# Optimization experiments

Measured on AMD Instinct MI355X. Metric: run time of the kernel, lower is better.

The kernel has to match this reference:

```python
import jax, jax.numpy as jnp
import numpy as np

N_STATE = 16
PNAMES = ['in_w', 'conv_w', 'conv_b', 'xproj_w', 'dt_w', 'dt_b', 'A_log', 'D', 'ln_g', 'ln_b', 'out_w']


def _ss2d_params(key, dm, K):
    di = 2 * dm                       # expand = 2
    dr = (dm + 15) // 16              # dt_rank = ceil(d_model/16)
    ks = jax.random.split(key, 6)
    s = lambda k, shape, sc: jax.random.normal(k, shape, jnp.float32) * sc
    cshape = (di, 1, 3, 3) if K == 4 else (di, 1, 3)   # depthwise conv kernel
    return {
        'in_w': s(ks[0], (2 * di, dm), dm ** -0.5),
        'conv_w': s(ks[1], cshape, 0.3),
        'conv_b': jnp.zeros((di,), jnp.float32),
        'xproj_w': s(ks[2], (K, dr + 2 * N_STATE, di), di ** -0.5),
        'dt_w': s(ks[3], (K, di, dr), dr ** -0.5),
        'dt_b': s(ks[4], (K, di), 0.1),
        'A_log': jnp.log(jnp.arange(1, N_STATE + 1, dtype=jnp.float32)) * jnp.ones((K, di, N_STATE), jnp.float32),
        'D': jnp.ones((K, di), jnp.float32),
        'ln_g': jnp.ones((di,), jnp.float32),
        'ln_b': jnp.zeros((di,), jnp.float32),
        'out_w': s(ks[5], (dm, di), di ** -0.5),
    }


def _ln(x, g, b, eps=1e-5):
    m = jnp.mean(x, -1, keepdims=True)
    v = jnp.mean((x - m) ** 2, -1, keepdims=True)
    return (x - m) * jax.lax.rsqrt(v + eps) * g + b


def _scan_branches(xs, p):
    # xs: (B, K, di, L) -- selective scan along L for each direction k
    dr = p['dt_w'].shape[-1]
    x_dbl = jnp.einsum('bkdl,kcd->bkcl', xs, p['xproj_w'])
    dts, Bs, Cs = jnp.split(x_dbl, [dr, dr + N_STATE], axis=2)
    delta = jax.nn.softplus(jnp.einsum('bkrl,kdr->bkdl', dts, p['dt_w']) + p['dt_b'][None, :, :, None])
    A = -jnp.exp(p['A_log'])                               # (K, di, N)
    dA = jnp.exp(jnp.einsum('bkdl,kdn->lbkdn', delta, A))  # time-major for scan
    dBu = jnp.einsum('bkdl,bknl,bkdl->lbkdn', delta, Bs, xs)

    def step(h, io):
        a, bu = io
        h = a * h + bu
        return h, h

    h0 = jnp.zeros(dA.shape[1:], xs.dtype)
    _, hs = jax.lax.scan(step, h0, (dA, dBu))              # (L, B, K, di, N)
    y = jnp.einsum('lbkdn,bknl->bkdl', hs, Cs)
    return y + xs * p['D'][None, :, :, None]


def _ss2d_2d(x, p):
    # VMamba SS2D: x (B, H, W, dm) -> (B, H, W, dm), 4 scan directions
    xz = jnp.einsum('bhwc,ec->bhwe', x, p['in_w'])
    xin, z = jnp.split(xz, 2, -1)
    u = xin.transpose(0, 3, 1, 2)
    u = jax.lax.conv_general_dilated(u, p['conv_w'], (1, 1), 'SAME',
        dimension_numbers=('NCHW', 'OIHW', 'NCHW'), feature_group_count=u.shape[1])
    u = jax.nn.silu(u + p['conv_b'][None, :, None, None])
    Bb, di, H, W = u.shape
    L = H * W
    xf = u.reshape(Bb, di, L)                              # row-major
    xt = u.transpose(0, 1, 3, 2).reshape(Bb, di, L)        # col-major
    xs = jnp.stack([xf, xt, xf[..., ::-1], xt[..., ::-1]], 1)
    ys = _scan_branches(xs, p)                             # (B, 4, di, L)
    y0 = ys[:, 0]
    y2 = ys[:, 2][..., ::-1]
    y1 = ys[:, 1].reshape(Bb, di, W, H).transpose(0, 1, 3, 2).reshape(Bb, di, L)
    y3 = ys[:, 3][..., ::-1].reshape(Bb, di, W, H).transpose(0, 1, 3, 2).reshape(Bb, di, L)
    y = (y0 + y1 + y2 + y3).transpose(0, 2, 1).reshape(Bb, H, W, di)
    y = _ln(y, p['ln_g'], p['ln_b']) * jax.nn.silu(z)
    return jnp.einsum('bhwe,ce->bhwc', y, p['out_w'])


def _ss2d_1d(x, p):
    # SS2D_xb fuse block: x (B, L, dm) -> (B, L, dm), bidirectional 1D scan
    xz = jnp.einsum('blc,ec->ble', x, p['in_w'])
    xin, z = jnp.split(xz, 2, -1)
    u = xin.transpose(0, 2, 1)
    u = jax.lax.conv_general_dilated(u, p['conv_w'], (1,), 'SAME',
        dimension_numbers=('NCH', 'OIH', 'NCH'), feature_group_count=u.shape[1])
    u = jax.nn.silu(u + p['conv_b'][None, :, None])
    xs = jnp.stack([u, u[..., ::-1]], 1)                   # K = 2
    ys = _scan_branches(xs, p)
    y = (ys[:, 0] + ys[:, 1][..., ::-1]).transpose(0, 2, 1)
    y = _ln(y, p['ln_g'], p['ln_b']) * jax.nn.silu(z)
    return jnp.einsum('ble,ce->blc', y, p['out_w'])


def _bridge(C1, C2, C3, p1, p2, p3, pf, n1_g, n1_b):
    y1 = _ss2d_2d(C1.transpose(0, 2, 3, 1), p1).transpose(0, 3, 1, 2)
    y2 = _ss2d_2d(C2.transpose(0, 2, 3, 1), p2).transpose(0, 3, 1, 2)
    y3 = _ss2d_2d(C3.transpose(0, 2, 3, 1), p3).transpose(0, 3, 1, 2)
    B_, C, H, W = y1.shape                                 # C=24, H=W=112
    # faithful RAW reshapes (no permute), exactly as the torch source does
    F1 = y1.reshape(B_, H * W, C)
    F2 = y2.reshape(B_, H * W // 2, C)
    F3 = y3.reshape(B_, H * W // 4, C)
    F = jnp.concatenate([F1, F2, F3], axis=1)              # (B, 21952, 24)
    F = F + _ss2d_1d(_ln(F, n1_g, n1_b), pf)               # dropout = identity (eval)
    o1 = F[:, :12544, :].reshape(B_, C, H, W)
    o2 = F[:, 12544:18816, :].reshape(B_, C * 2, H // 2, W // 2)
    o3 = F[:, 18816:, :].reshape(B_, C * 4, H // 4, W // 4)
    return (o1, o2, o3)


def setup_inputs() -> dict:
    key = jax.random.key(0)
    ks = jax.random.split(key, 7)
    inp = {
        'C1': jax.random.normal(ks[0], (1, 24, 112, 112), jnp.float32),
        'C2': jax.random.normal(ks[1], (1, 48, 56, 56), jnp.float32),
        'C3': jax.random.normal(ks[2], (1, 96, 28, 28), jnp.float32),
    }
    for pfx, dm, K, kk in [('m1', 24, 4, ks[3]), ('m2', 48, 4, ks[4]), ('m3', 96, 4, ks[5]), ('fz', 24, 2, ks[6])]:
        p = _ss2d_params(kk, dm, K)
        for n in PNAMES:
            inp[pfx + '_' + n] = p[n]
    inp['n1_g'] = jnp.ones((24,), jnp.float32)
    inp['n1_b'] = jnp.zeros((24,), jnp.float32)
    return inp


def reference(C1, C2, C3, m1_in_w, m1_conv_w, m1_conv_b, m1_xproj_w, m1_dt_w, m1_dt_b, m1_A_log, m1_D, m1_ln_g, m1_ln_b, m1_out_w, m2_in_w, m2_conv_w, m2_conv_b, m2_xproj_w, m2_dt_w, m2_dt_b, m2_A_log, m2_D, m2_ln_g, m2_ln_b, m2_out_w, m3_in_w, m3_conv_w, m3_conv_b, m3_xproj_w, m3_dt_w, m3_dt_b, m3_A_log, m3_D, m3_ln_g, m3_ln_b, m3_out_w, fz_in_w, fz_conv_w, fz_conv_b, fz_xproj_w, fz_dt_w, fz_dt_b, fz_A_log, fz_D, fz_ln_g, fz_ln_b, fz_out_w, n1_g, n1_b):
    p1 = dict(zip(PNAMES, (m1_in_w, m1_conv_w, m1_conv_b, m1_xproj_w, m1_dt_w, m1_dt_b, m1_A_log, m1_D, m1_ln_g, m1_ln_b, m1_out_w)))
    p2 = dict(zip(PNAMES, (m2_in_w, m2_conv_w, m2_conv_b, m2_xproj_w, m2_dt_w, m2_dt_b, m2_A_log, m2_D, m2_ln_g, m2_ln_b, m2_out_w)))
    p3 = dict(zip(PNAMES, (m3_in_w, m3_conv_w, m3_conv_b, m3_xproj_w, m3_dt_w, m3_dt_b, m3_A_log, m3_D, m3_ln_g, m3_ln_b, m3_out_w)))
    pf = dict(zip(PNAMES, (fz_in_w, fz_conv_w, fz_conv_b, fz_xproj_w, fz_dt_w, fz_dt_b, fz_A_log, fz_D, fz_ln_g, fz_ln_b, fz_out_w)))
    return _bridge(C1, C2, C3, p1, p2, p3, pf, n1_g, n1_b)
```

## Files before the change

kernel.cpp:

```cpp
#include <hip/hip_runtime.h>
#include <hip/hip_bf16.h>
#include <hip/hip_fp16.h>

#define NST 16
#define L2E 1.4426950408889634f

typedef const void* inp;
typedef __half h16;

struct Job {
  inp Cin;
  inp in_w, conv_w, conv_b, xproj_w, dt_w, dt_b, A_log, D, ln_g, ln_b, out_w;
  h16 *u_pre, *z, *u, *delta, *Bs, *Cs, *yg;
  h16 *Hc;
  float *yacc, *Wc, *bc, *Ssum, *A2t, *F0out;
  float *outF; const float* resid;
  const int* aflg;
  int dm, di, dr, K, H, W, L, NCH, CLEN, is2d, TL, CG, PT, cinf;
};
struct Jobs { Job j[4]; int n; const int* dtf; };

__device__ __forceinline__ float ldw(inp p, size_t i, int f32){
  return f32 ? ((const float*)p)[i]
             : __bfloat162float(((const __hip_bfloat16*)p)[i]);
}
__device__ __forceinline__ float hf(const h16* p, size_t i){ return __half2float(p[i]); }
__device__ __forceinline__ float sigm(float x){ return 1.0f/(1.0f + __expf(-x)); }
__device__ __forceinline__ float silu_(float x){ return x * sigm(x); }
__device__ __forceinline__ float softp(float x){ return (x > 20.0f) ? x : __logf(1.0f + __expf(x)); }

__device__ __forceinline__ int map_pos(const Job& J, int k, int l){
  int rev   = J.is2d ? (k >= 2) : (k == 1);
  int trans = J.is2d ? (k & 1) : 0;
  int sl = rev ? (J.L - 1 - l) : l;
  return trans ? ((sl % J.H)*J.W + sl / J.H) : sl;
}

union F4H { float4 f; __half2 h[4]; };

__device__ __forceinline__ void ld16v(const h16* p, float* o){
  const float4* q = (const float4*)p;
  F4H a, b; a.f = q[0]; b.f = q[1];
  #pragma unroll
  for (int i = 0; i < 4; i++){ float2 x = __half22float2(a.h[i]); o[2*i] = x.x; o[2*i+1] = x.y; }
  #pragma unroll
  for (int i = 0; i < 4; i++){ float2 x = __half22float2(b.h[i]); o[8+2*i] = x.x; o[8+2*i+1] = x.y; }
}

__device__ __forceinline__ void ld8v(const h16* p, float* o){
  F4H a; a.f = *(const float4*)p;
  #pragma unroll
  for (int i = 0; i < 4; i++){ float2 x = __half22float2(a.h[i]); o[2*i] = x.x; o[2*i+1] = x.y; }
}

__device__ __forceinline__ void cvt16(float4 a4, float4 b4, float* o){
  F4H a, b; a.f = a4; b.f = b4;
  #pragma unroll
  for (int i = 0; i < 4; i++){ float2 x = __half22float2(a.h[i]); o[2*i] = x.x; o[2*i+1] = x.y; }
  #pragma unroll
  for (int i = 0; i < 4; i++){ float2 x = __half22float2(b.h[i]); o[8+2*i] = x.x; o[8+2*i+1] = x.y; }
}


__global__ void k_detect(const unsigned* D1, int* flag, int* afl){
  if (blockIdx.x == 0){
    if (threadIdx.x == 0) flag[0] = (D1[0] == 0x3F800000u) ? 1 : 0;
    if (threadIdx.x < 4) afl[threadIdx.x] = 1;
  }
}

__global__ void k_wcomb(Jobs js){
  int f32 = *js.dtf;
  int b = blockIdx.x;
  for (int m = 0; m < js.n; m++){
    const Job& J = js.j[m];
    int CC = J.di + 2*NST;
    int CC2 = CC + NST;
    int tot = J.K * CC2 * J.di;
    int nb = (tot + 255) >> 8;
    if (b < nb){
      int t = (b << 8) + (int)threadIdx.x;
      if (t < tot){
        int d = t % J.di; int r = t / J.di; int cout = r % CC2; int k = r / CC2;
        if (cout < J.di){
          float v = 0.0f;
          for (int rr = 0; rr < J.dr; rr++)
            v += ldw(J.dt_w, (size_t)(k*J.di + cout)*J.dr + rr, f32) *
                 ldw(J.xproj_w, (size_t)(k*(J.dr + 2*NST) + rr)*J.di + d, f32);
          J.Wc[(size_t)(k*CC + cout)*J.di + d] = v;
          if (d == 0) J.bc[k*CC + cout] = ldw(J.dt_b, k*J.di + cout, f32);
        } else if (cout < CC){
          int nn = cout - J.di;
          J.Wc[(size_t)(k*CC + cout)*J.di + d] =
            ldw(J.xproj_w, (size_t)(k*(J.dr + 2*NST) + J.dr + nn)*J.di + d, f32);
          if (d == 0) J.bc[k*CC + cout] = 0.0f;
        } else {
          int nn = cout - CC;
          float v = -L2E*__expf(ldw(J.A_log, ((size_t)(k*J.di + d) << 4) + nn, f32));
          J.A2t[(size_t)(k*NST + nn)*J.di + d] = v;
          float base = -L2E*__expf(ldw(J.A_log, ((size_t)(k*J.di + d) << 4), f32));
          float expect = (float)(nn+1)*base;
          if (fabsf(v - expect) > 1e-4f*fabsf(expect) + 1e-6f)
            atomicAnd((int*)J.aflg, 0);
        }
      }
      return;
    }
    b -= nb;
  }
}

__global__ void k_inproj(Jobs js){
  int f32 = *js.dtf;
  int b = blockIdx.x;
  for (int m = 0; m < js.n; m++){
    const Job& J = js.j[m];
    int tot = 2*J.di*J.L;
    int nb = (tot + 255) >> 8;
    if (b < nb){
      int cf = J.cinf ? 1 : f32;
      int t = (b << 8) + (int)threadIdx.x;
      if (t < tot){
        int p = t % J.L; int e = t / J.L;
        float acc;
        if (cf && f32){
          const float* Ci = (const float*)J.Cin;
          const float4* w4 = (const float4*)((const float*)J.in_w + (size_t)e*J.dm);
          float a0 = 0.f, a1 = 0.f, a2 = 0.f, a3 = 0.f;
          int n4 = J.dm >> 2;
          for (int c4 = 0; c4 < n4; c4++){
            float4 w = w4[c4];
            int c = c4 << 2;
            a0 = fmaf(Ci[(size_t)(c+0)*J.L + p], w.x, a0);
            a1 = fmaf(Ci[(size_t)(c+1)*J.L + p], w.y, a1);
            a2 = fmaf(Ci[(size_t)(c+2)*J.L + p], w.z, a2);
            a3 = fmaf(Ci[(size_t)(c+3)*J.L + p], w.w, a3);
          }
          acc = (a0+a1)+(a2+a3);
        } else {
          float a0 = 0.f, a1 = 0.f, a2 = 0.f, a3 = 0.f;
          for (int c = 0; c < J.dm; c += 4){
            a0 = fmaf(ldw(J.Cin, (size_t)(c+0)*J.L + p, cf), ldw(J.in_w, (size_t)e*J.dm + c+0, f32), a0);
            a1 = fmaf(ldw(J.Cin, (size_t)(c+1)*J.L + p, cf), ldw(J.in_w, (size_t)e*J.dm + c+1, f32), a1);
            a2 = fmaf(ldw(J.Cin, (size_t)(c+2)*J.L + p, cf), ldw(J.in_w, (size_t)e*J.dm + c+2, f32), a2);
            a3 = fmaf(ldw(J.Cin, (size_t)(c+3)*J.L + p, cf), ldw(J.in_w, (size_t)e*J.dm + c+3, f32), a3);
          }
          acc = (a0+a1)+(a2+a3);
        }
        if (e < J.di) J.u_pre[(size_t)p*J.di + e] = __float2half(acc);
        else          J.z[(size_t)p*J.di + (e - J.di)] = __float2half(acc);
      }
      return;
    }
    b -= nb;
  }
}

__global__ __launch_bounds__(256) void k_lnproj(const float* F0, inp g, inp bb, inp in_w,
                                                h16* u_pre, h16* z, int L, const int* dtf){
  __shared__ float xr[64][25];
  __shared__ float wsmT[24*96];
  int f32 = *dtf;
  int p0 = blockIdx.x << 6;
  int rows = L - p0; if (rows > 64) rows = 64;
  for (int i = threadIdx.x; i < 24*96; i += 256){
    int c = i / 96, e = i % 96;
    wsmT[i] = ldw(in_w, (size_t)e*24 + c, f32);
  }
  for (int idx = threadIdx.x; idx < rows*24; idx += 256){
    int r = idx / 24, c = idx % 24;
    xr[r][c] = F0[(size_t)(p0 + r)*24 + c];
  }
  __syncthreads();
  if ((int)threadIdx.x < rows){
    float* row = xr[threadIdx.x];
    float s = 0.f;
    #pragma unroll
    for (int c = 0; c < 24; c++) s += row[c];
    float mean = s * (1.0f/24.0f);
    float s2 = 0.f;
    #pragma unroll
    for (int c = 0; c < 24; c++){ float t = row[c]-mean; s2 = fmaf(t,t,s2); }
    float rs = rsqrtf(s2*(1.0f/24.0f) + 1e-5f);
    #pragma unroll
    for (int c = 0; c < 24; c++)
      row[c] = (row[c]-mean)*rs*ldw(g,c,f32) + ldw(bb,c,f32);
  }
  __syncthreads();
  for (int idx = threadIdx.x; idx < rows*96; idx += 256){
    int r = idx / 96, e = idx % 96;
    const float* row = xr[r];
    float acc = 0.f;
    #pragma unroll
    for (int c = 0; c < 24; c++) acc = fmaf(row[c], wsmT[c*96 + e], acc);
    if (e < 48) u_pre[(size_t)(p0+r)*48 + e] = __float2half(acc);
    else        z[(size_t)(p0+r)*48 + (e-48)] = __float2half(acc);
  }
}

__global__ void k_conv(Jobs js){
  int f32 = *js.dtf;
  int b = blockIdx.x;
  for (int m = 0; m < js.n; m++){
    const Job& J = js.j[m];
    int tot = J.L * J.di;
    int nb = (tot + 255) >> 8;
    if (b < nb){
      int t = (b << 8) + (int)threadIdx.x;
      if (t < tot){
        int d = t % J.di; int p = t / J.di;
        float acc = ldw(J.conv_b, d, f32);
        if (J.is2d){
          int h = p / J.W, w = p % J.W;
          for (int kh = 0; kh < 3; kh++){
            int hh = h + kh - 1;
            if ((unsigned)hh < (unsigned)J.H){
              for (int kw = 0; kw < 3; kw++){
                int ww = w + kw - 1;
                if ((unsigned)ww < (unsigned)J.W)
                  acc += ldw(J.conv_w, d*9 + kh*3 + kw, f32) * hf(J.u_pre, (size_t)(hh*J.W + ww)*J.di + d);
              }
            }
          }
        } else {
          for (int kk = 0; kk < 3; kk++){
            int pp = p + kk - 1;
            if ((unsigned)pp < (unsigned)J.L)
              acc += ldw(J.conv_w, d*3 + kk, f32) * hf(J.u_pre, (size_t)pp*J.di + d);
          }
        }
        J.u[(size_t)p*J.di + d] = __float2half(silu_(acc));
      }
      return;
    }
    b -= nb;
  }
}

__global__ void k_deltaBC(Jobs js){
  extern __shared__ float xt[];
  int b = blockIdx.x;
  for (int m = 0; m < js.n; m++){
    const Job& J = js.j[m];
    int TL = J.TL;
    int ntile = (J.L + TL - 1)/TL;
    int nb = J.K * ntile;
    if (b < nb){
      int k = b / ntile, tile = b % ntile;
      int l0 = tile * TL;
      int stride = J.di + 4;
      int d8n = J.di >> 3;
      int VE = TL * d8n;
      for (int idx = threadIdx.x; idx < VE; idx += 256){
        int ll = idx / d8n, d8 = idx % d8n;
        int l = l0 + ll;
        float o[8];
        if (l < J.L){
          ld8v(J.u + (size_t)map_pos(J, k, l)*J.di + (d8 << 3), o);
        } else {
          for (int i = 0; i < 8; i++) o[i] = 0.0f;
        }
        float4* dst = (float4*)(xt + ll*stride + (d8 << 3));
        dst[0] = make_float4(o[0],o[1],o[2],o[3]);
        dst[1] = make_float4(o[4],o[5],o[6],o[7]);
      }
      __syncthreads();
      int CC = J.di + 2*NST;
      int c4n = CC >> 2;
      int NL4 = TL >> 2;
      int items = NL4 * c4n;
      int n4 = J.di >> 2;
      for (int item = threadIdx.x; item < items; item += 256){
        int l4 = item % NL4;
        int cbase = (item / NL4) << 2;
        const float4* w0 = (const float4*)(J.Wc + (size_t)(k*CC + cbase+0)*J.di);
        const float4* w1 = (const float4*)(J.Wc + (size_t)(k*CC + cbase+1)*J.di);
        const float4* w2 = (const float4*)(J.Wc + (size_t)(k*CC + cbase+2)*J.di);
        const float4* w3 = (const float4*)(J.Wc + (size_t)(k*CC + cbase+3)*J.di);
        const float4* x0 = (const float4*)(xt + (l4 + 0*NL4)*stride);
        const float4* x1 = (const float4*)(xt + (l4 + 1*NL4)*stride);
        const float4* x2 = (const float4*)(xt + (l4 + 2*NL4)*stride);
        const float4* x3 = (const float4*)(xt + (l4 + 3*NL4)*stride);
        float acc[4][4];
        #pragma unroll
        for (int j = 0; j < 4; j++){
          acc[j][0]=0.f; acc[j][1]=0.f; acc[j][2]=0.f; acc[j][3]=0.f;
        }
        #pragma unroll 4
        for (int d4 = 0; d4 < n4; d4++){
          float4 W0 = w0[d4], W1 = w1[d4], W2 = w2[d4], W3 = w3[d4];
          float4 X0 = x0[d4], X1 = x1[d4], X2 = x2[d4], X3 = x3[d4];
          #define DOT4(a,X,W) { a = fmaf(X.x,W.x,a); a = fmaf(X.y,W.y,a); a = fmaf(X.z,W.z,a); a = fmaf(X.w,W.w,a); }
          DOT4(acc[0][0],X0,W0) DOT4(acc[0][1],X0,W1) DOT4(acc[0][2],X0,W2) DOT4(acc[0][3],X0,W3)
          DOT4(acc[1][0],X1,W0) DOT4(acc[1][1],X1,W1) DOT4(acc[1][2],X1,W2) DOT4(acc[1][3],X1,W3)
          DOT4(acc[2][0],X2,W0) DOT4(acc[2][1],X2,W1) DOT4(acc[2][2],X2,W2) DOT4(acc[2][3],X2,W3)
          DOT4(acc[3][0],X3,W0) DOT4(acc[3][1],X3,W1) DOT4(acc[3][2],X3,W2) DOT4(acc[3][3],X3,W3)
          #undef DOT4
        }
        float b0 = J.bc[k*CC + cbase+0], b1 = J.bc[k*CC + cbase+1];
        float b2 = J.bc[k*CC + cbase+2], b3 = J.bc[k*CC + cbase+3];
        #pragma unroll
        for (int j = 0; j < 4; j++){
          int l = l0 + l4 + NL4*j;
          if (l >= J.L) continue;
          float av[4] = {acc[j][0]+b0, acc[j][1]+b1, acc[j][2]+b2, acc[j][3]+b3};
          #pragma unroll
          for (int i = 0; i < 4; i++){
            int cout = cbase + i; float v = av[i];
            if (cout < J.di)            J.delta[((size_t)k*J.L + l)*J.di + cout] = __float2half(softp(v));
            else if (cout < J.di + NST) J.Bs[((size_t)k*J.L + l)*NST + (cout - J.di)] = __float2half(v);
            else                        J.Cs[((size_t)k*J.L + l)*NST + (cout - J.di - NST)] = __float2half(v);
          }
        }
      }
      return;
    }
    b -= nb;
  }
}

#define STEPRQ { if (rev){ if(--rm < 0){ rm = J.H - 1; qd--; } } else { if(++rm == J.H){ rm = 0; qd++; } } }

#define HUPD_GEN(S, DX, B) { \
  _Pragma("unroll") \
  for (int n = 0; n < NST; n++) h[n] = fmaf(exp2f((S) * A2[n]), h[n], (DX) * (B)[n]); }
#define HUPDY_GEN(S, DX, B, C, Y) { \
  _Pragma("unroll") \
  for (int n = 0; n < NST; n++){ h[n] = fmaf(exp2f((S) * A2[n]), h[n], (DX) * (B)[n]); (Y) = fmaf(h[n], (C)[n], (Y)); } }

#define POWTREE(Q, P) \
  float P[NST]; \
  P[0]=(Q); P[1]=P[0]*P[0]; P[2]=P[1]*P[0]; P[3]=P[1]*P[1]; \
  P[4]=P[3]*P[0]; P[5]=P[3]*P[1]; P[6]=P[3]*P[2]; P[7]=P[3]*P[3]; \
  P[8]=P[7]*P[0]; P[9]=P[7]*P[1]; P[10]=P[7]*P[2]; P[11]=P[7]*P[3]; \
  P[12]=P[7]*P[4]; P[13]=P[7]*P[5]; P[14]=P[7]*P[6]; P[15]=P[7]*P[7];

#define HUPD_POW(S, DX, B) { \
  float q_ = exp2f((S) * A0); \
  POWTREE(q_, Pw) \
  _Pragma("unroll") \
  for (int n = 0; n < NST; n++) h[n] = fmaf(Pw[n], h[n], (DX) * (B)[n]); }
#define HUPDY_POW(S, DX, B, C, Y) { \
  float q_ = exp2f((S) * A0); \
  POWTREE(q_, Pw) \
  _Pragma("unroll") \
  for (int n = 0; n < NST; n++){ h[n] = fmaf(Pw[n], h[n], (DX) * (B)[n]); (Y) = fmaf(h[n], (C)[n], (Y)); } }

__global__ __launch_bounds__(256) void k_passA(Jobs js){
  int b = blockIdx.x;
  int wid = (int)threadIdx.x >> 6;
  int lane = (int)threadIdx.x & 63;
  for (int m = 0; m < js.n; m++){
    const Job& J = js.j[m];
    int DG = (J.di + 63) >> 6;
    int units = J.K * J.NCH * DG;
    int nb = (units + 3) >> 2;
    if (b < nb){
      int uu = (b << 2) + wid;
      if (uu >= units) return;
      int afl = *J.aflg;
      int k = uu / (J.NCH * DG);
      int r = uu % (J.NCH * DG);
      int chunk = r / DG, dg = r % DG;
      int d = (dg << 6) + lane;
      if (d >= J.di) return;
      int c0 = chunk * J.CLEN;
      int c1 = c0 + J.CLEN; if (c1 > J.L) c1 = J.L;
      size_t sb = (size_t)(k*J.NCH + chunk);
      if (c0 >= J.L){
        J.Ssum[sb*J.di + d] = 0.0f;
        #pragma unroll
        for (int n = 0; n < NST; n++) J.Hc[(sb*NST + n)*J.di + d] = __float2half(0.0f);
        return;
      }
      float h[NST];
      #pragma unroll
      for (int n = 0; n < NST; n++) h[n] = 0.0f;
      float ss = 0.0f;
      int rev   = J.is2d ? (k >= 2) : (k == 1);
      int trans = J.is2d ? (k & 1) : 0;
      int rm = 0, qd = 0;
      if (trans){
        int sl0 = rev ? (J.L - 1 - c0) : c0;
        qd = sl0 / J.H; rm = sl0 % J.H;
      }
      const h16* dlt = J.delta + ((size_t)k*J.L)*J.di + d;
      const h16* Bb  = J.Bs + ((size_t)k*J.L)*NST;
      if (afl){
        float A0 = J.A2t[(size_t)(k*NST)*J.di + d];
        int l = c0;
        int pos0;
        h16 s0h, s1h, x0h, x1h;
        float4 B0a, B0b, B1a, B1b;
        if (trans){ pos0 = rm*J.W + qd; STEPRQ; } else pos0 = rev ? (J.L-1-l) : l;
        s0h = dlt[(size_t)l*J.di];
        x0h = J.u[(size_t)pos0*J.di + d];
        { const float4* bp = (const float4*)(Bb + (size_t)l*NST); B0a = bp[0]; B0b = bp[1]; }
        s1h = s0h; x1h = x0h; B1a = B0a; B1b = B0b;
        if (l + 1 < c1){
          int pos1;
          if (trans){ pos1 = rm*J.W + qd; STEPRQ; } else pos1 = rev ? (J.L-2-l) : (l+1);
          s1h = dlt[(size_t)(l+1)*J.di];
          x1h = J.u[(size_t)pos1*J.di + d];
          const float4* bq = (const float4*)(Bb + (size_t)(l+1)*NST); B1a = bq[0]; B1b = bq[1];
        }
        while (l < c1){
          int ln = l + 2;
          h16 ns0 = s0h, ns1 = s1h, nx0 = x0h, nx1 = x1h;
          float4 nB0a = B0a, nB0b = B0b, nB1a = B1a, nB1b = B1b;
          if (ln < c1){
            int np0;
            if (trans){ np0 = rm*J.W + qd; STEPRQ; } else np0 = rev ? (J.L-1-ln) : ln;
            ns0 = dlt[(size_t)ln*J.di];
            nx0 = J.u[(size_t)np0*J.di + d];
            const float4* bp = (const float4*)(Bb + (size_t)ln*NST); nB0a = bp[0]; nB0b = bp[1];
            if (ln + 1 < c1){
              int np1;
              if (trans){ np1 = rm*J.W + qd; STEPRQ; } else np1 = rev ? (J.L-2-ln) : (ln+1);
              ns1 = dlt[(size_t)(ln+1)*J.di];
              nx1 = J.u[(size_t)np1*J.di + d];
              const float4* bq = (const float4*)(Bb + (size_t)(ln+1)*NST); nB1a = bq[0]; nB1b = bq[1];
            }
          }
          {
            float s0 = __half2float(s0h), x0 = __half2float(x0h);
            float B0[NST]; cvt16(B0a, B0b, B0);
            float dx0 = s0 * x0; ss += s0;
            HUPD_POW(s0, dx0, B0)
            if (l + 1 < c1){
              float s1 = __half2float(s1h), x1 = __half2float(x1h);
              float B1[NST]; cvt16(B1a, B1b, B1);
              float dx1 = s1 * x1; ss += s1;
              HUPD_POW(s1, dx1, B1)
            }
          }
          l = ln;
          s0h = ns0; s1h = ns1; x0h = nx0; x1h = nx1;
          B0a = nB0a; B0b = nB0b; B1a = nB1a; B1b = nB1b;
        }
      } else {
        float A2[NST];
        #pragma unroll
        for (int n = 0; n < NST; n++) A2[n] = J.A2t[(size_t)(k*NST + n)*J.di + d];
        for (int l = c0; l < c1; l++){
          int pos;
          if (trans){ pos = rm*J.W + qd; STEPRQ; } else pos = rev ? (J.L-1-l) : l;
          float s0 = hf(dlt, (size_t)l*J.di);
          float x0 = hf(J.u, (size_t)pos*J.di + d);
          float B0[NST]; ld16v(Bb + (size_t)l*NST, B0);
          float dx0 = s0 * x0; ss += s0;
          HUPD_GEN(s0, dx0, B0)
        }
      }
      J.Ssum[sb*J.di + d] = ss;
      #pragma unroll
      for (int n = 0; n < NST; n++)
        J.Hc[(sb*NST + n)*J.di + d] = __float2half(h[n]);
      return;
    }
    b -= nb;
  }
}

__global__ __launch_bounds__(1024) void k_passB(Jobs js){
  __shared__ float sA[64*17], sH[64*17];
  int b = blockIdx.x;
  int sid = (int)threadIdx.x >> 4;
  int dd  = (int)threadIdx.x & 15;
  for (int m = 0; m < js.n; m++){
    const Job& J = js.j[m];
    int DT = J.di >> 4;
    int nb = J.K * NST * DT;
    if (b < nb){
      int k  = b / (NST*DT);
      int r  = b % (NST*DT);
      int n  = r / DT;
      int dt = r % DT;
      int d = dt*16 + dd;
      int SL = J.NCH >> 6;
      int c0 = sid*SL, c1 = c0 + SL;
      float An = J.A2t[(size_t)(k*NST + n)*J.di + d];
      float a = 1.0f, hagg = 0.0f;
      {
        size_t rb = (size_t)(k*J.NCH + c0);
        float ss = J.Ssum[rb*J.di + d];
        h16 hch  = J.Hc[(rb*NST + n)*J.di + d];
        for (int c = c0; c < c1; c++){
          float ssc = ss; h16 hcc = hch;
          if (c + 1 < c1){
            size_t rn = (size_t)(k*J.NCH + c + 1);
            ss  = J.Ssum[rn*J.di + d];
            hch = J.Hc[(rn*NST + n)*J.di + d];
          }
          float P = exp2f(An * ssc);
          hagg = fmaf(P, hagg, __half2float(hcc));
          a *= P;
        }
      }
      sA[sid*17+dd] = a; sH[sid*17+dd] = hagg;
      __syncthreads();
      #pragma unroll
      for (int s = 1; s < 64; s <<= 1){
        float pa = 1.0f, ph = 0.0f;
        if (sid >= s){ pa = sA[(sid-s)*17+dd]; ph = sH[(sid-s)*17+dd]; }
        __syncthreads();
        hagg = fmaf(a, ph, hagg);
        a *= pa;
        sA[sid*17+dd] = a; sH[sid*17+dd] = hagg;
        __syncthreads();
      }
      float Hp = (sid == 0) ? 0.0f : sH[(sid-1)*17+dd];
      {
        size_t rb = (size_t)(k*J.NCH + c0);
        float ss = J.Ssum[rb*J.di + d];
        h16 hch  = J.Hc[(rb*NST + n)*J.di + d];
        for (int c = c0; c < c1; c++){
          float ssc = ss; float hc = __half2float(hch);
          size_t idx = ((size_t)(k*J.NCH + c)*NST + n)*J.di + d;
          if (c + 1 < c1){
            size_t rn = (size_t)(k*J.NCH + c + 1);
            ss  = J.Ssum[rn*J.di + d];
            hch = J.Hc[(rn*NST + n)*J.di + d];
          }
          float P = exp2f(An * ssc);
          J.Hc[idx] = __float2half(Hp);
          Hp = fmaf(P, Hp, hc);
        }
      }
      return;
    }
    b -= nb;
  }
}

__global__ __launch_bounds__(256) void k_passC(Jobs js){
  int f32 = *js.dtf;
  int b = blockIdx.x;
  int wid = (int)threadIdx.x >> 6;
  int lane = (int)threadIdx.x & 63;
  for (int m = 0; m < js.n; m++){
    const Job& J = js.j[m];
    int DG = (J.di + 63) >> 6;
    int units = J.K * J.NCH * DG;
    int nb = (units + 3) >> 2;
    if (b < nb){
      int uu = (b << 2) + wid;
      if (uu >= units) return;
      int afl = *J.aflg;
      int k = uu / (J.NCH * DG);
      int r = uu % (J.NCH * DG);
      int chunk = r / DG, dg = r % DG;
      int d = (dg << 6) + lane;
      if (d >= J.di) return;
      int c0 = chunk * J.CLEN;
      int c1 = c0 + J.CLEN; if (c1 > J.L) c1 = J.L;
      if (c0 >= J.L) return;
      float h[NST];
      size_t sb = (size_t)(k*J.NCH + chunk);
      #pragma unroll
      for (int n = 0; n < NST; n++) h[n] = hf(J.Hc, (sb*NST + n)*J.di + d);
      float Dd = ldw(J.D, k*J.di + d, f32);
      float* yk = J.yacc + (size_t)k*J.L*J.di;
      int rev   = J.is2d ? (k >= 2) : (k == 1);
      int trans = J.is2d ? (k & 1) : 0;
      int rm = 0, qd = 0;
      if (trans){
        int sl0 = rev ? (J.L - 1 - c0) : c0;
        qd = sl0 / J.H; rm = sl0 % J.H;
      }
      const h16* dlt = J.delta + ((size_t)k*J.L)*J.di + d;
      const h16* Bb  = J.Bs + ((size_t)k*J.L)*NST;
      const h16* Cb  = J.Cs + ((size_t)k*J.L)*NST;
      if (afl){
        float A0 = J.A2t[(size_t)(k*NST)*J.di + d];
        int l = c0;
        int pos0, pos1 = 0;
        h16 s0h, s1h, x0h, x1h;
        float4 B0a, B0b, B1a, B1b, C0a, C0b, C1a, C1b;
        if (trans){ pos0 = rm*J.W + qd; STEPRQ; } else pos0 = rev ? (J.L-1-l) : l;
        s0h = dlt[(size_t)l*J.di];
        x0h = J.u[(size_t)pos0*J.di + d];
        { const float4* bp = (const float4*)(Bb + (size_t)l*NST); B0a = bp[0]; B0b = bp[1];
          const float4* cp = (const float4*)(Cb + (size_t)l*NST); C0a = cp[0]; C0b = cp[1]; }
        s1h = s0h; x1h = x0h; B1a = B0a; B1b = B0b; C1a = C0a; C1b = C0b;
        if (l + 1 < c1){
          if (trans){ pos1 = rm*J.W + qd; STEPRQ; } else pos1 = rev ? (J.L-2-l) : (l+1);
          s1h = dlt[(size_t)(l+1)*J.di];
          x1h = J.u[(size_t)pos1*J.di + d];
          const float4* bq = (const float4*)(Bb + (size_t)(l+1)*NST); B1a = bq[0]; B1b = bq[1];
          const float4* cq = (const float4*)(Cb + (size_t)(l+1)*NST); C1a = cq[0]; C1b = cq[1];
        }
        while (l < c1){
          int ln = l + 2;
          int np0 = pos0, np1 = pos1;
          h16 ns0 = s0h, ns1 = s1h, nx0 = x0h, nx1 = x1h;
          float4 nB0a = B0a, nB0b = B0b, nB1a = B1a, nB1b = B1b;
          float4 nC0a = C0a, nC0b = C0b, nC1a = C1a, nC1b = C1b;
          if (ln < c1){
            if (trans){ np0 = rm*J.W + qd; STEPRQ; } else np0 = rev ? (J.L-1-ln) : ln;
            ns0 = dlt[(size_t)ln*J.di];
            nx0 = J.u[(size_t)np0*J.di + d];
            { const float4* bp = (const float4*)(Bb + (size_t)ln*NST); nB0a = bp[0]; nB0b = bp[1];
              const float4* cp = (const float4*)(Cb + (size_t)ln*NST); nC0a = cp[0]; nC0b = cp[1]; }
            if (ln + 1 < c1){
              if (trans){ np1 = rm*J.W + qd; STEPRQ; } else np1 = rev ? (J.L-2-ln) : (ln+1);
              ns1 = dlt[(size_t)(ln+1)*J.di];
              nx1 = J.u[(size_t)np1*J.di + d];
              const float4* bq = (const float4*)(Bb + (size_t)(ln+1)*NST); nB1a = bq[0]; nB1b = bq[1];
              const float4* cq = (const float4*)(Cb + (size_t)(ln+1)*NST); nC1a = cq[0]; nC1b = cq[1];
            }
          }
          {
            float s0 = __half2float(s0h), x0 = __half2float(x0h);
            float B0[NST], C0[NST]; cvt16(B0a, B0b, B0); cvt16(C0a, C0b, C0);
            float dx0 = s0 * x0;
            float y0 = 0.0f;
            HUPDY_POW(s0, dx0, B0, C0, y0)
            y0 = fmaf(Dd, x0, y0);
            yk[(size_t)pos0*J.di + d] = y0;
            if (l + 1 < c1){
              float s1 = __half2float(s1h), x1 = __half2float(x1h);
              float B1[NST], C1[NST]; cvt16(B1a, B1b, B1); cvt16(C1a, C1b, C1);
              float dx1 = s1 * x1;
              float y1 = 0.0f;
              HUPDY_POW(s1, dx1, B1, C1, y1)
              y1 = fmaf(Dd, x1, y1);
              yk[(size_t)pos1*J.di + d] = y1;
            }
          }
          l = ln; pos0 = np0; pos1 = np1;
          s0h = ns0; s1h = ns1; x0h = nx0; x1h = nx1;
          B0a = nB0a; B0b = nB0b; B1a = nB1a; B1b = nB1b;
          C0a = nC0a; C0b = nC0b; C1a = nC1a; C1b = nC1b;
        }
      } else {
        float A2[NST];
        #pragma unroll
        for (int n = 0; n < NST; n++) A2[n] = J.A2t[(size_t)(k*NST + n)*J.di + d];
        for (int l = c0; l < c1; l++){
          int pos;
          if (trans){ pos = rm*J.W + qd; STEPRQ; } else pos = rev ? (J.L-1-l) : l;
          float s0 = hf(dlt, (size_t)l*J.di);
          float x0 = hf(J.u, (size_t)pos*J.di + d);
          float B0[NST], C0[NST];
          ld16v(Bb + (size_t)l*NST, B0);
          ld16v(Cb + (size_t)l*NST, C0);
          float dx0 = s0 * x0;
          float y0 = 0.0f;
          HUPDY_GEN(s0, dx0, B0, C0, y0)
          y0 = fmaf(Dd, x0, y0);
          yk[(size_t)pos*J.di + d] = y0;
        }
      }
      return;
    }
    b -= nb;
  }
}

__global__ void k_merge(Jobs js){
  extern __shared__ float sm[];
  int f32 = *js.dtf;
  int b = blockIdx.x;
  for (int m = 0; m < js.n; m++){
    const Job& J = js.j[m];
    int nbk = (J.L + J.PT - 1)/J.PT;
    if (b < nbk){
      int di = J.di, PT = J.PT;
      int st = di + 1, st2 = di + 2;
      int p0 = b * PT;
      int rows = J.L - p0; if (rows > PT) rows = PT;
      float* ya = sm;
      h16*   zz = (h16*)(sm + (size_t)PT*st);
      float* mres = (float*)(zz + (size_t)PT*st2);
      float* owT = mres + 2*PT;
      size_t LD = (size_t)J.L*di;
      int tot = rows*di;
      for (int idx = threadIdx.x; idx < tot; idx += 256){
        int r = idx / di, d = idx % di;
        size_t pp = (size_t)p0*di + idx;
        float v = J.yacc[pp];
        for (int k = 1; k < J.K; k++) v += J.yacc[(size_t)k*LD + pp];
        ya[r*st + d] = v;
        zz[r*st2 + d] = J.z[pp];
      }
      if (J.outF){
        for (int idx = threadIdx.x; idx < J.dm*di; idx += 256){
          int c = idx / di, e = idx % di;
          owT[e*25 + c] = ldw(J.out_w, (size_t)c*di + e, f32);
        }
      }
      __syncthreads();
      int wid = (int)threadIdx.x >> 6, lane = (int)threadIdx.x & 63;
      for (int r = wid; r < rows; r += 4){
        float s = 0.0f, s2 = 0.0f;
        for (int d = lane; d < di; d += 64){
          float v = ya[r*st + d];
          s += v; s2 = fmaf(v, v, s2);
        }
        for (int o = 32; o > 0; o >>= 1){
          s  += __shfl_down(s, o);
          s2 += __shfl_down(s2, o);
        }
        if (lane == 0){
          float mean = s / di;
          float var = s2/di - mean*mean;
          mres[r] = mean;
          mres[PT + r] = rsqrtf(var + 1e-5f);
        }
      }
      __syncthreads();
      if (J.outF){
        {
          int r = (int)threadIdx.x & (PT - 1);
          int dgrp = (int)threadIdx.x / PT;
          int G = 256 / PT;
          if (r < rows){
            float mean = mres[r], rs = mres[PT + r];
            for (int d = dgrp; d < di; d += G){
              float ln = (ya[r*st + d] - mean)*rs*ldw(J.ln_g, d, f32) + ldw(J.ln_b, d, f32);
              ya[r*st + d] = ln * silu_(__half2float(zz[r*st2 + d]));
            }
          }
        }
        __syncthreads();
        for (int idx = threadIdx.x; idx < rows*J.dm; idx += 256){
          int r = idx / J.dm, c = idx % J.dm;
          const float* lr = ya + r*st;
          float acc = 0.0f;
          for (int e = 0; e < di; e += 8){
            #pragma unroll
            for (int j = 0; j < 8; j++)
              acc = fmaf(lr[e+j], owT[(e+j)*25 + c], acc);
          }
          size_t o = (size_t)(p0 + r)*J.dm + c;
          J.outF[o] = J.resid[o] + acc;
        }
      } else {
        int r = (int)threadIdx.x & (PT - 1);
        int dgrp = (int)threadIdx.x / PT;
        int G = 256 / PT;
        if (r < rows){
          float mean = mres[r], rs = mres[PT + r];
          int p = p0 + r;
          for (int d = dgrp; d < di; d += G){
            float ln = (ya[r*st + d] - mean)*rs*ldw(J.ln_g, d, f32) + ldw(J.ln_b, d, f32);
            J.yg[(size_t)d*J.L + p] = __float2half(ln * silu_(__half2float(zz[r*st2 + d])));
          }
        }
      }
      return;
    }
    b -= nbk;
  }
}

__global__ void k_outproj(Jobs js){
  int f32 = *js.dtf;
  int b = blockIdx.x;
  for (int m = 0; m < js.n; m++){
    const Job& J = js.j[m];
    int tot = J.dm * J.L;
    int nb = (tot + 255) >> 8;
    if (b < nb){
      int t = (b << 8) + (int)threadIdx.x;
      if (t < tot){
        int p = t % J.L; int c = t / J.L;
        float acc = 0.0f;
        for (int e = 0; e < J.di; e += 8){
          #pragma unroll
          for (int j = 0; j < 8; j++)
            acc = fmaf(hf(J.yg, (size_t)(e+j)*J.L + p),
                       ldw(J.out_w, (size_t)c*J.di + e + j, f32), acc);
        }
        J.F0out[(size_t)c*J.L + p] = acc;
      }
      return;
    }
    b -= nb;
  }
}

static inline int cdiv_i(int a, int b){ return (a + b - 1)/b; }

extern "C" void kernel_launch(void* const* d_in, const int* in_sizes, int n_in,
                              void* d_out, int out_size, void* d_ws, size_t ws_size,
                              hipStream_t stream){
  (void)in_sizes; (void)n_in; (void)out_size; (void)ws_size;
  char* base = (char*)d_ws;
  size_t off = 0;
  auto alloc = [&](size_t bytes)->char*{
    off = (off + 255) & ~(size_t)255;
    char* p = base + off; off += bytes; return p;
  };

  int*   dtf = (int*)alloc(4);
  int*   afl = (int*)alloc(4*4);
  float* F0  = (float*)alloc(526848u*4);
  float* Wc1 = (float*)alloc(4u*80*48*4);   float* bc1 = (float*)alloc(4u*80*4);
  float* Wc2 = (float*)alloc(4u*128*96*4);  float* bc2 = (float*)alloc(4u*128*4);
  float* Wc3 = (float*)alloc(4u*224*192*4); float* bc3 = (float*)alloc(4u*224*4);
  float* Wcf = (float*)alloc(2u*80*48*4);   float* bcf = (float*)alloc(2u*80*4);
  float* A21 = (float*)alloc(4u*NST*48*4);
  float* A22 = (float*)alloc(4u*NST*96*4);
  float* A23 = (float*)alloc(4u*NST*192*4);
  float* A2f = (float*)alloc(2u*NST*48*4);
  size_t regionA = off;

  auto fill = [&](Job& J, int pbase, inp Cin, int cinf,
                  int dm, int di, int dr, int K, int H, int W, int L,
                  int NCH, int CLEN, int is2d, int TL, int PT,
                  float* Wc, float* bc, float* A2t, float* F0out){
    J.Cin = Cin; J.cinf = cinf;
    J.in_w    = d_in[pbase+0];
    J.conv_w  = d_in[pbase+1];
    J.conv_b  = d_in[pbase+2];
    J.xproj_w = d_in[pbase+3];
    J.dt_w    = d_in[pbase+4];
    J.dt_b    = d_in[pbase+5];
    J.A_log   = d_in[pbase+6];
    J.D       = d_in[pbase+7];
    J.ln_g    = d_in[pbase+8];
    J.ln_b    = d_in[pbase+9];
    J.out_w   = d_in[pbase+10];
    size_t LD = (size_t)L*di;
    J.yacc  = (float*)alloc((size_t)K*LD*4);
    J.u_pre = (h16*)J.yacc;
    J.z     = (h16*)alloc(LD*2);
    J.u     = (h16*)alloc(LD*2);
    J.yg    = J.u;
    J.delta = (h16*)alloc((size_t)K*LD*2);
    J.Bs    = (h16*)alloc((size_t)K*L*NST*2);
    J.Cs    = (h16*)alloc((size_t)K*L*NST*2);
    J.Hc    = (h16*)alloc((size_t)K*NCH*NST*di*2);
    J.Ssum  = (float*)alloc((size_t)K*NCH*di*4);
    J.Wc = Wc; J.bc = bc; J.A2t = A2t; J.F0out = F0out;
    J.outF = nullptr; J.resid = nullptr;
    J.dm=dm; J.di=di; J.dr=dr; J.K=K; J.H=H; J.W=W; J.L=L; J.NCH=NCH; J.CLEN=CLEN;
    J.is2d=is2d; J.TL=TL; J.CG=256/TL; J.PT=PT;
  };

  Jobs js3; js3.n = 3; js3.dtf = dtf;
  fill(js3.j[0],  3, d_in[0], 0, 24,  48, 2, 4, 112, 112, 12544, 1024, 13, 1, 64, 32, Wc1, bc1, A21, F0);
  fill(js3.j[1], 14, d_in[1], 0, 48,  96, 3, 4,  56,  56,  3136,  256, 13, 1, 32, 32, Wc2, bc2, A22, F0 + 301056);
  fill(js3.j[2], 25, d_in[2], 0, 96, 192, 6, 4,  28,  28,   784,   64, 13, 1, 16, 16, Wc3, bc3, A23, F0 + 451584);
  js3.j[0].aflg = afl + 0;
  js3.j[1].aflg = afl + 1;
  js3.j[2].aflg = afl + 2;

  off = regionA;
  Jobs js1; js1.n = 1; js1.dtf = dtf;
  fill(js1.j[0], 36, nullptr, 1, 24, 48, 2, 2, 21952, 1, 21952, 2048, 11, 0, 64, 32, Wcf, bcf, A2f, nullptr);
  js1.j[0].aflg = afl + 3;
  js1.j[0].outF = (float*)d_out;
  js1.j[0].resid = F0;

  Jobs js4; js4.n = 4; js4.dtf = dtf;
  js4.j[0] = js3.j[0]; js4.j[1] = js3.j[1]; js4.j[2] = js3.j[2]; js4.j[3] = js1.j[0];

  auto grids = [&](const Jobs& js, int which)->int{
    int g = 0;
    for (int m = 0; m < js.n; m++){
      const Job& J = js.j[m];
      switch (which){
        case 0: g += cdiv_i(J.K*(J.di+3*NST)*J.di, 256); break;
        case 1: g += cdiv_i(2*J.di*J.L, 256); break;
        case 2: g += cdiv_i(J.L*J.di, 256); break;
        case 3: g += J.K * cdiv_i(J.L, J.TL); break;
        case 4: g += cdiv_i(J.K * J.NCH * cdiv_i(J.di, 64), 4); break;
        case 5: g += J.K * NST * (J.di >> 4); break;
        case 6: g += cdiv_i(J.L, J.PT); break;
        case 7: g += cdiv_i(J.dm*J.L, 256); break;
      }
    }
    return g;
  };
  auto shm_dbc = [&](const Jobs& js)->int{
    int s = 0;
    for (int m = 0; m < js.n; m++){ int v = js.j[m].TL*(js.j[m].di+4)*4; if (v > s) s = v; }
    return s;
  };
  auto shm_merge = [&](const Jobs& js)->int{
    int s = 0;
    for (int m = 0; m < js.n; m++){
      const Job& J = js.j[m];
      int v = J.PT*(J.di+1)*4 + J.PT*(J.di+2)*2 + 2*J.PT*4 + (J.outF ? 48*25*4 : 0);
      if (v > s) s = v;
    }
    return s;
  };

  k_detect <<<1, 64, 0, stream>>>((const unsigned*)d_in[10], dtf, afl);

  k_wcomb  <<<grids(js4,0), 256, 0, stream>>>(js4);
  k_inproj <<<grids(js3,1), 256, 0, stream>>>(js3);
  k_conv   <<<grids(js3,2), 256, 0, stream>>>(js3);
  k_deltaBC<<<grids(js3,3), 256, shm_dbc(js3), stream>>>(js3);
  k_passA  <<<grids(js3,4), 256, 0, stream>>>(js3);
  k_passB  <<<grids(js3,5), 1024, 0, stream>>>(js3);
  k_passC  <<<grids(js3,4), 256, 0, stream>>>(js3);
  k_merge  <<<grids(js3,6), 256, shm_merge(js3), stream>>>(js3);
  k_outproj<<<grids(js3,7), 256, 0, stream>>>(js3);

  k_lnproj <<<cdiv_i(21952,64), 256, 0, stream>>>(F0, d_in[47], d_in[48], d_in[36],
                                                  js1.j[0].u_pre, js1.j[0].z, 21952, dtf);
  k_conv   <<<grids(js1,2), 256, 0, stream>>>(js1);
  k_deltaBC<<<grids(js1,3), 256, shm_dbc(js1), stream>>>(js1);
  k_passA  <<<grids(js1,4), 256, 0, stream>>>(js1);
  k_passB  <<<grids(js1,5), 1024, 0, stream>>>(js1);
  k_passC  <<<grids(js1,4), 256, 0, stream>>>(js1);
  k_merge  <<<grids(js1,6), 256, shm_merge(js1), stream>>>(js1);
}
```

Baseline: 469.0 us.

## Fuse out-projection into merge kernel and stage deltaBC outputs through shared memory

The separate k_outproj kernel is removed, and its output projection now runs inside k_merge on the gated LayerNorm rows already held in shared memory. This drops the fp16 yg round trip through global memory and one kernel launch. k_deltaBC now writes its delta/B/C results to a shared-memory tile first and then stores them to global memory in coalesced 8-byte vectors, instead of scattered 2-byte stores. The jobs are also reordered so the large-di, small-L stage is scheduled first. The cost is more shared memory per block in deltaBC and out_w reads from global memory inside the merge blocks.

```diff
diff --git a/kernel.cpp b/kernel.cpp
--- a/kernel.cpp
+++ b/kernel.cpp
@@ -11,7 +11,7 @@
 struct Job {
   inp Cin;
   inp in_w, conv_w, conv_b, xproj_w, dt_w, dt_b, A_log, D, ln_g, ln_b, out_w;
-  h16 *u_pre, *z, *u, *delta, *Bs, *Cs, *yg;
+  h16 *u_pre, *z, *u, *delta, *Bs, *Cs;
   h16 *Hc;
   float *yacc, *Wc, *bc, *Ssum, *A2t, *F0out;
   float *outF; const float* resid;
@@ -249,6 +249,8 @@
       int k = b / ntile, tile = b % ntile;
       int l0 = tile * TL;
       int stride = J.di + 4;
+      int CC = J.di + 2*NST;
+      h16* yout = (h16*)(xt + (size_t)TL*stride);
       int d8n = J.di >> 3;
       int VE = TL * d8n;
       for (int idx = threadIdx.x; idx < VE; idx += 256){
@@ -265,7 +267,6 @@
         dst[1] = make_float4(o[4],o[5],o[6],o[7]);
       }
       __syncthreads();
-      int CC = J.di + 2*NST;
       int c4n = CC >> 2;
       int NL4 = TL >> 2;
       int items = NL4 * c4n;
@@ -299,19 +300,31 @@
         }
         float b0 = J.bc[k*CC + cbase+0], b1 = J.bc[k*CC + cbase+1];
         float b2 = J.bc[k*CC + cbase+2], b3 = J.bc[k*CC + cbase+3];
+        int dosp = (cbase < J.di);
         #pragma unroll
         for (int j = 0; j < 4; j++){
-          int l = l0 + l4 + NL4*j;
-          if (l >= J.L) continue;
+          int ll = l4 + NL4*j;
           float av[4] = {acc[j][0]+b0, acc[j][1]+b1, acc[j][2]+b2, acc[j][3]+b3};
+          h16* yo = yout + ll*CC + cbase;
           #pragma unroll
-          for (int i = 0; i < 4; i++){
-            int cout = cbase + i; float v = av[i];
-            if (cout < J.di)            J.delta[((size_t)k*J.L + l)*J.di + cout] = __float2half(softp(v));
-            else if (cout < J.di + NST) J.Bs[((size_t)k*J.L + l)*NST + (cout - J.di)] = __float2half(v);
-            else                        J.Cs[((size_t)k*J.L + l)*NST + (cout - J.di - NST)] = __float2half(v);
-          }
-        }
+          for (int i = 0; i < 4; i++)
+            yo[i] = __float2half(dosp ? softp(av[i]) : av[i]);
+        }
+      }
+      __syncthreads();
+      int WI = TL * c4n;
+      for (int idx = threadIdx.x; idx < WI; idx += 256){
+        int ll = idx / c4n, c4 = idx % c4n;
+        int l = l0 + ll;
+        if (l >= J.L) continue;
+        int cbase = c4 << 2;
+        uint2 v = *(const uint2*)(yout + ll*CC + cbase);
+        if (cbase < J.di)
+          *(uint2*)(J.delta + ((size_t)k*J.L + l)*J.di + cbase) = v;
+        else if (cbase < J.di + NST)
+          *(uint2*)(J.Bs + ((size_t)k*J.L + l)*NST + (cbase - J.di)) = v;
+        else
+          *(uint2*)(J.Cs + ((size_t)k*J.L + l)*NST + (cbase - J.di - NST)) = v;
       }
       return;
     }
@@ -710,20 +723,20 @@
         }
       }
       __syncthreads();
+      {
+        int r = (int)threadIdx.x & (PT - 1);
+        int dgrp = (int)threadIdx.x / PT;
+        int G = 256 / PT;
+        if (r < rows){
+          float mean = mres[r], rs = mres[PT + r];
+          for (int d = dgrp; d < di; d += G){
+            float ln = (ya[r*st + d] - mean)*rs*ldw(J.ln_g, d, f32) + ldw(J.ln_b, d, f32);
+            ya[r*st + d] = ln * silu_(__half2float(zz[r*st2 + d]));
+          }
+        }
+      }
+      __syncthreads();
       if (J.outF){
-        {
-          int r = (int)threadIdx.x & (PT - 1);
-          int dgrp = (int)threadIdx.x / PT;
-          int G = 256 / PT;
-          if (r < rows){
-            float mean = mres[r], rs = mres[PT + r];
-            for (int d = dgrp; d < di; d += G){
-              float ln = (ya[r*st + d] - mean)*rs*ldw(J.ln_g, d, f32) + ldw(J.ln_b, d, f32);
-              ya[r*st + d] = ln * silu_(__half2float(zz[r*st2 + d]));
-            }
-          }
-        }
-        __syncthreads();
         for (int idx = threadIdx.x; idx < rows*J.dm; idx += 256){
           int r = idx / J.dm, c = idx % J.dm;
           const float* lr = ya + r*st;
@@ -737,47 +750,22 @@
           J.outF[o] = J.resid[o] + acc;
         }
       } else {
-        int r = (int)threadIdx.x & (PT - 1);
-        int dgrp = (int)threadIdx.x / PT;
-        int G = 256 / PT;
-        if (r < rows){
-          float mean = mres[r], rs = mres[PT + r];
-          int p = p0 + r;
-          for (int d = dgrp; d < di; d += G){
-            float ln = (ya[r*st + d] - mean)*rs*ldw(J.ln_g, d, f32) + ldw(J.ln_b, d, f32);
-            J.yg[(size_t)d*J.L + p] = __float2half(ln * silu_(__half2float(zz[r*st2 + d])));
-          }
+        for (int idx = threadIdx.x; idx < PT*J.dm; idx += 256){
+          int r = idx % PT, c = idx / PT;
+          if (r >= rows) continue;
+          const float* lr = ya + r*st;
+          float acc = 0.0f;
+          for (int e = 0; e < di; e += 8){
+            #pragma unroll
+            for (int j = 0; j < 8; j++)
+              acc = fmaf(lr[e+j], ldw(J.out_w, (size_t)c*di + e + j, f32), acc);
+          }
+          J.F0out[(size_t)c*J.L + p0 + r] = acc;
         }
       }
       return;
     }
     b -= nbk;
-  }
-}
-
-__global__ void k_outproj(Jobs js){
-  int f32 = *js.dtf;
-  int b = blockIdx.x;
-  for (int m = 0; m < js.n; m++){
-    const Job& J = js.j[m];
-    int tot = J.dm * J.L;
-    int nb = (tot + 255) >> 8;
-    if (b < nb){
-      int t = (b << 8) + (int)threadIdx.x;
-      if (t < tot){
-        int p = t % J.L; int c = t / J.L;
-        float acc = 0.0f;
-        for (int e = 0; e < J.di; e += 8){
-          #pragma unroll
-          for (int j = 0; j < 8; j++)
-            acc = fmaf(hf(J.yg, (size_t)(e+j)*J.L + p),
-                       ldw(J.out_w, (size_t)c*J.di + e + j, f32), acc);
-        }
-        J.F0out[(size_t)c*J.L + p] = acc;
-      }
-      return;
-    }
-    b -= nb;
   }
 }
 
@@ -828,7 +816,6 @@
     J.u_pre = (h16*)J.yacc;
     J.z     = (h16*)alloc(LD*2);
     J.u     = (h16*)alloc(LD*2);
-    J.yg    = J.u;
     J.delta = (h16*)alloc((size_t)K*LD*2);
     J.Bs    = (h16*)alloc((size_t)K*L*NST*2);
     J.Cs    = (h16*)alloc((size_t)K*L*NST*2);
@@ -841,9 +828,9 @@
   };
 
   Jobs js3; js3.n = 3; js3.dtf = dtf;
-  fill(js3.j[0],  3, d_in[0], 0, 24,  48, 2, 4, 112, 112, 12544, 1024, 13, 1, 64, 32, Wc1, bc1, A21, F0);
+  fill(js3.j[0], 25, d_in[2], 0, 96, 192, 6, 4,  28,  28,   784,   64, 13, 1, 16, 16, Wc3, bc3, A23, F0 + 451584);
   fill(js3.j[1], 14, d_in[1], 0, 48,  96, 3, 4,  56,  56,  3136,  256, 13, 1, 32, 32, Wc2, bc2, A22, F0 + 301056);
-  fill(js3.j[2], 25, d_in[2], 0, 96, 192, 6, 4,  28,  28,   784,   64, 13, 1, 16, 16, Wc3, bc3, A23, F0 + 451584);
+  fill(js3.j[2],  3, d_in[0], 0, 24,  48, 2, 4, 112, 112, 12544, 1024, 13, 1, 64, 32, Wc1, bc1, A21, F0);
   js3.j[0].aflg = afl + 0;
   js3.j[1].aflg = afl + 1;
   js3.j[2].aflg = afl + 2;
@@ -870,14 +857,17 @@
         case 4: g += cdiv_i(J.K * J.NCH * cdiv_i(J.di, 64), 4); break;
         case 5: g += J.K * NST * (J.di >> 4); break;
         case 6: g += cdiv_i(J.L, J.PT); break;
-        case 7: g += cdiv_i(J.dm*J.L, 256); break;
       }
     }
     return g;
   };
   auto shm_dbc = [&](const Jobs& js)->int{
     int s = 0;
-    for (int m = 0; m < js.n; m++){ int v = js.j[m].TL*(js.j[m].di+4)*4; if (v > s) s = v; }
+    for (int m = 0; m < js.n; m++){
+      const Job& J = js.j[m];
+      int v = J.TL*(J.di+4)*4 + J.TL*(J.di+2*NST)*2;
+      if (v > s) s = v;
+    }
     return s;
   };
   auto shm_merge = [&](const Jobs& js)->int{
@@ -900,7 +890,6 @@
   k_passB  <<<grids(js3,5), 1024, 0, stream>>>(js3);
   k_passC  <<<grids(js3,4), 256, 0, stream>>>(js3);
   k_merge  <<<grids(js3,6), 256, shm_merge(js3), stream>>>(js3);
-  k_outproj<<<grids(js3,7), 256, 0, stream>>>(js3);
 
   k_lnproj <<<cdiv_i(21952,64), 256, 0, stream>>>(F0, d_in[47], d_in[48], d_in[36],
                                                   js1.j[0].u_pre, js1.j[0].z, 21952, dtf);
```

Result: slower. 481.8 us (+2.7%).
